# Optimization experiments

Measured on AMD Instinct MI355X. Metric: run time of the kernel, lower is better.

## Reference

```python
import jax, jax.numpy as jnp
import numpy as np

I, H, L, O = 128, 512, 2, 1  # input_size, hidden_size, num_layers, output_size
B, S = 64, 512


def setup_inputs() -> dict:
    key = jax.random.key(0)
    ks = jax.random.split(key, 12)
    inp = {
        "x": jax.random.normal(ks[0], (B, S, I), dtype=jnp.float32),
        "theta": jax.random.normal(ks[1], (I, H), dtype=jnp.float32) * 0.02,
        "phi": jax.random.normal(ks[2], (I, H), dtype=jnp.float32) * 0.02,
        "theta_noise": jax.random.normal(ks[3], (I, H), dtype=jnp.float32) * 0.01,
        "phi_noise": jax.random.normal(ks[4], (I, H), dtype=jnp.float32) * 0.01,
        # stacked per-layer LSTM weights (all layers take H-dim input)
        "W_ih": jax.random.normal(ks[5], (L, 4 * H, H), dtype=jnp.float32) * (1.0 / np.sqrt(H)),
        "W_hh": jax.random.normal(ks[6], (L, 4 * H, H), dtype=jnp.float32) * (1.0 / np.sqrt(H)),
        "b_ih": jax.random.normal(ks[7], (L, 4 * H), dtype=jnp.float32) * (1.0 / np.sqrt(H)),
        "b_hh": jax.random.normal(ks[8], (L, 4 * H), dtype=jnp.float32) * (1.0 / np.sqrt(H)),
        "fc1_w": jax.random.normal(ks[9], (H, H), dtype=jnp.float32) * (1.0 / np.sqrt(H)),
        "fc1_b": jnp.zeros((H,), dtype=jnp.float32),
        "fc2_w": jax.random.normal(ks[10], (O, H), dtype=jnp.float32) * (1.0 / np.sqrt(H)),
        "fc2_b": jnp.zeros((O,), dtype=jnp.float32),
    }
    return inp


def _lstm_layer(xs, Wih, Whh, bih, bhh):
    # xs: (S, B, H) -> hs: (S, B, H). PyTorch gate order: i, f, g, o.
    Bn = xs.shape[1]
    Hn = Whh.shape[1]
    # precompute input projections for all timesteps in one GEMM
    x_proj = jnp.einsum("sbh,gh->sbg", xs, Wih) + bih + bhh  # (S, B, 4H)

    def step(carry, xp):
        h, c = carry
        gates = xp + h @ Whh.T  # (B, 4H)
        i, f, g, o = jnp.split(gates, 4, axis=-1)
        i = jax.nn.sigmoid(i)
        f = jax.nn.sigmoid(f)
        g = jnp.tanh(g)
        o = jax.nn.sigmoid(o)
        c = f * c + i * g
        h = o * jnp.tanh(c)
        return (h, c), h

    h0 = jnp.zeros((Bn, Hn), dtype=xs.dtype)
    c0 = jnp.zeros((Bn, Hn), dtype=xs.dtype)
    _, hs = jax.lax.scan(step, (h0, c0), x_proj)
    return hs


def reference(x, theta, phi, theta_noise, phi_noise, W_ih, W_hh, b_ih, b_hh,
              fc1_w, fc1_b, fc2_w, fc2_b):
    # QuantumInspiredLayer: |x @ (cos(theta+n) + i*sin(phi+n))| done as two real GEMMs
    real = jnp.einsum("bsi,ih->bsh", x, jnp.cos(theta + theta_noise))
    imag = jnp.einsum("bsi,ih->bsh", x, jnp.sin(phi + phi_noise))
    q = jnp.sqrt(real * real + imag * imag)  # (B, S, H)

    hs = jnp.transpose(q, (1, 0, 2))  # (S, B, H)
    n_layers = W_ih.shape[0]
    for l in range(n_layers):
        hs = _lstm_layer(hs, W_ih[l], W_hh[l], b_ih[l], b_hh[l])
    last = hs[-1]  # (B, H) -- out[:, -1, :]

    h1 = jax.nn.relu(last @ fc1_w.T + fc1_b)
    # dropout is identity in eval mode
    return h1 @ fc2_w.T + fc2_b  # (B, O)
```

## Files before the change

kernel.cpp:

```cpp
#include <hip/hip_runtime.h>


typedef _Float16 f16;
typedef _Float16 f16x8 __attribute__((ext_vector_type(8)));
typedef float f32x4 __attribute__((ext_vector_type(4)));
typedef unsigned long long u64;

#define MFMA16(a, b, c) __builtin_amdgcn_mfma_f32_16x16x32_f16((a), (b), (c), 0, 0, 0)
#define LD_AG(p) __hip_atomic_load((p), __ATOMIC_RELAXED, __HIP_MEMORY_SCOPE_AGENT)
#define ST_AG(p, v) __hip_atomic_store((p), (v), __ATOMIC_RELAXED, __HIP_MEMORY_SCOPE_AGENT)

#define OFF_Q16 0UL
#define OFF_X16 33554432UL
#define OFF_W16 41943040UL
#define OFF_COS 50331648UL
#define OFF_SIN 50462720UL
#define OFF_BSUM 50593792UL
#define OFF_HBUF 50610176UL
#define OFF_HLAST 51003392UL
#define OFF_FC1WT 51134464UL
#define OFF_FLG 52183040UL
#define WS_NEEDED 52215808UL

__global__ __launch_bounds__(256) void k_prep(
    const float* __restrict__ x, const float* __restrict__ theta,
    const float* __restrict__ phi, const float* __restrict__ thn,
    const float* __restrict__ phn, const float* __restrict__ Wih,
    const float* __restrict__ Whh, const float* __restrict__ bih,
    const float* __restrict__ bhh, const float* __restrict__ fc1w,
    f16* __restrict__ x16, f16* __restrict__ w16, f16* __restrict__ cosT,
    f16* __restrict__ sinT, float* __restrict__ bsum, float* __restrict__ fc1wT,
    f16* __restrict__ hbuf, unsigned* __restrict__ flg) {
  const int T1 = 4194304;
  const int T2 = T1 + 4194304;
  const int T3 = T2 + 65536;
  const int T4 = T3 + 262144;
  const int T5 = T4 + 4096;
  const int T6 = T5 + 196608;
  const int T7 = T6 + 8192;
  for (int idx = blockIdx.x * 256 + threadIdx.x; idx < T7; idx += gridDim.x * 256) {
    if (idx < T1) {
      int s = idx >> 13, rem = idx & 8191, b = rem >> 7, i = rem & 127;
      x16[idx] = (f16)x[b * 65536 + s * 128 + i];
    } else if (idx < T2) {
      int j = idx - T1;
      int l = j >> 21, rem = j & 2097151, r = rem >> 10, k = rem & 1023;
      float v = (k < 512) ? Wih[((size_t)l * 2048 + r) * 512 + k]
                          : Whh[((size_t)l * 2048 + r) * 512 + (k - 512)];
      w16[(size_t)l * 2097152 + (size_t)r * 1024 + k] = (f16)v;
    } else if (idx < T3) {
      int e = idx - T2;
      int i = e >> 9, h = e & 511;
      cosT[h * 128 + i] = (f16)cosf(theta[e] + thn[e]);
      sinT[h * 128 + i] = (f16)sinf(phi[e] + phn[e]);
    } else if (idx < T4) {
      int e = idx - T3;
      int n = e >> 9, k = e & 511;
      fc1wT[k * 512 + n] = fc1w[e];
    } else if (idx < T5) {
      int e = idx - T4;
      bsum[e] = bih[e] + bhh[e];
    } else if (idx < T6) {
      hbuf[idx - T5] = (f16)0.f;
    } else {
      flg[idx - T6] = 0u;
    }
  }
}

__global__ __launch_bounds__(256) void k_quantum(
    const f16* __restrict__ x16, const f16* __restrict__ cosT,
    const f16* __restrict__ sinT, f16* __restrict__ q16) {
  __shared__ __align__(16) f16 a_lds[64 * 136];
  const int tid = threadIdx.x;
  const int r0 = blockIdx.x * 64, h0 = blockIdx.y * 128;
#pragma unroll
  for (int g = 0; g < 4; ++g) {
    int G = g * 256 + tid, row = G >> 4, col = G & 15;
    *(uint4*)((char*)a_lds + row * 272 + col * 16) =
        *(const uint4*)(x16 + (size_t)(r0 + row) * 128 + col * 8);
  }
  __syncthreads();
  const int wv = tid >> 6, lane = tid & 63, n15 = lane & 15, quad = lane >> 4;
  const int nb = h0 + wv * 32;
  f32x4 ac[4][2], as_[4][2];
#pragma unroll
  for (int mt = 0; mt < 4; ++mt)
#pragma unroll
    for (int nt = 0; nt < 2; ++nt) {
      ac[mt][nt] = (f32x4){0.f, 0.f, 0.f, 0.f};
      as_[mt][nt] = (f32x4){0.f, 0.f, 0.f, 0.f};
    }
#pragma unroll
  for (int it = 0; it < 4; ++it) {
    f16x8 a[4];
#pragma unroll
    for (int mt = 0; mt < 4; ++mt)
      a[mt] = *(const f16x8*)((const char*)a_lds + (mt * 16 + n15) * 272 + it * 64 + quad * 16);
#pragma unroll
    for (int nt = 0; nt < 2; ++nt) {
      const f16x8 bc = *(const f16x8*)(cosT + (size_t)(nb + nt * 16 + n15) * 128 + it * 32 + quad * 8);
      const f16x8 bs = *(const f16x8*)(sinT + (size_t)(nb + nt * 16 + n15) * 128 + it * 32 + quad * 8);
#pragma unroll
      for (int mt = 0; mt < 4; ++mt) {
        ac[mt][nt] = MFMA16(a[mt], bc, ac[mt][nt]);
        as_[mt][nt] = MFMA16(a[mt], bs, as_[mt][nt]);
      }
    }
  }
#pragma unroll
  for (int mt = 0; mt < 4; ++mt)
#pragma unroll
    for (int nt = 0; nt < 2; ++nt)
#pragma unroll
      for (int r = 0; r < 4; ++r) {
        int row = r0 + mt * 16 + quad * 4 + r;
        int col = nb + nt * 16 + n15;
        float re = ac[mt][nt][r], im = as_[mt][nt][r];
        q16[(size_t)row * 512 + col] = (f16)sqrtf(re * re + im * im);
      }
}

__device__ __forceinline__ f16x8 lds_a(const char* astage, int row, int it, int quad) {
  int pos = (it * 4 + quad) ^ (row & 7);
  return *(const f16x8*)(astage + row * 2048 + pos * 16);
}
__device__ __forceinline__ float sigf(float x) { return 1.f / (1.f + __expf(-x)); }
__device__ __forceinline__ float tanhf_fast(float x) { return 1.f - 2.f / (__expf(2.f * x) + 1.f); }

__global__ __launch_bounds__(512, 2) void k_rec(
    const f16* __restrict__ q16, const f16* __restrict__ w16,
    const float* __restrict__ bsum, f16* __restrict__ h0buf,
    f16* __restrict__ h1buf, float* __restrict__ hlast, unsigned* flg) {
  __shared__ __align__(16) char astage[32768];
  __shared__ float gbuf[16 * 132];

  const int tid = threadIdx.x, lane = tid & 63, wv = tid >> 6;
  const int n15 = lane & 15, quad = lane >> 4;
  const int qg = wv >> 1, ch = wv & 1;
  const int dom = blockIdx.x >> 5, role = blockIdx.x & 31;
  const int l = role >> 4, c0 = (role & 15) * 32;
  const int b0 = dom * 16;

  f16x8 wf[32];
  {
    const f16* wbase = w16 + ((size_t)l * 2048 + (size_t)(qg * 512 + c0 + ch * 16 + n15)) * 1024 + quad * 8;
#pragma unroll
    for (int it = 0; it < 32; ++it) wf[it] = *(const f16x8*)(wbase + it * 32);
  }
  float bb[4][2];
#pragma unroll
  for (int g = 0; g < 4; ++g)
#pragma unroll
    for (int j = 0; j < 2; ++j)
      bb[g][j] = bsum[l * 2048 + g * 512 + c0 + (tid & 15) * 2 + j];
  float cs0 = 0.f, cs1 = 0.f;

  unsigned* f0 = flg + (size_t)(dom * 2 + 0) * 1024;
  unsigned* f1 = flg + (size_t)(dom * 2 + 1) * 1024;
  unsigned* myflag = (l ? f1 : f0) + (size_t)(role & 15) * 64;
  const int pl = lane & 31;
  const unsigned* pollp = (pl < 16) ? (f0 + pl * 64) : (f1 + (pl - 16) * 64);

  const int srow = tid >> 5, scg = tid & 31;
  const int g0 = scg * 2;
  char* a_x0 = astage + srow * 2048 + ((g0 ^ (srow & 7)) * 16);
  char* a_x1 = astage + srow * 2048 + (((g0 + 1) ^ (srow & 7)) * 16);
  char* a_h0 = a_x0 + 1024;
  char* a_h1 = a_x1 + 1024;
  const size_t soff = (size_t)srow * 512 + scg * 16;
  const size_t h0base = (size_t)dom * 4 * 8192;
  const size_t h1base = (size_t)dom * 2 * 8192;

  for (int t = 0; t <= 511; ++t) {
    if (l == 0) {
      const f16* src = q16 + ((size_t)(t * 64 + b0 + srow)) * 512 + scg * 16;
      uint4 v0 = *(const uint4*)src;
      uint4 v1 = *(const uint4*)(src + 8);
      *(uint4*)a_x0 = v0;
      *(uint4*)a_x1 = v1;
    }
    if (t >= 1 || l == 1) {
      const int mytgt = (l == 0) ? ((pl < 16) ? t : (t - 2))
                                 : ((pl < 16) ? (t + 1) : t);
      while (true) {
        int f = (int)LD_AG(pollp);
        if (__all(f >= mytgt)) break;
        __builtin_amdgcn_s_sleep(1);
      }
    }
    if (l == 0) {
      const u64* hs0 = (const u64*)(h0buf + h0base + (size_t)((t - 1) & 3) * 8192 + soff);
      u64 x0 = LD_AG(hs0);
      u64 x1 = LD_AG(hs0 + 1);
      u64 x2 = LD_AG(hs0 + 2);
      u64 x3 = LD_AG(hs0 + 3);
      ((u64*)a_h0)[0] = x0; ((u64*)a_h0)[1] = x1;
      ((u64*)a_h1)[0] = x2; ((u64*)a_h1)[1] = x3;
    } else {
      const u64* hs0 = (const u64*)(h0buf + h0base + (size_t)(t & 3) * 8192 + soff);
      u64 x0 = LD_AG(hs0);
      u64 x1 = LD_AG(hs0 + 1);
      u64 x2 = LD_AG(hs0 + 2);
      u64 x3 = LD_AG(hs0 + 3);
      const u64* hs1 = (const u64*)(h1buf + h1base + (size_t)((t - 1) & 1) * 8192 + soff);
      u64 y0 = LD_AG(hs1);
      u64 y1 = LD_AG(hs1 + 1);
      u64 y2 = LD_AG(hs1 + 2);
      u64 y3 = LD_AG(hs1 + 3);
      ((u64*)a_x0)[0] = x0; ((u64*)a_x0)[1] = x1;
      ((u64*)a_x1)[0] = x2; ((u64*)a_x1)[1] = x3;
      ((u64*)a_h0)[0] = y0; ((u64*)a_h0)[1] = y1;
      ((u64*)a_h1)[0] = y2; ((u64*)a_h1)[1] = y3;
    }
    __syncthreads();

    f32x4 acc = (f32x4){0.f, 0.f, 0.f, 0.f};
#pragma unroll
    for (int it = 0; it < 32; ++it)
      acc = MFMA16(lds_a(astage, n15, it, quad), wf[it], acc);
#pragma unroll
    for (int r = 0; r < 4; ++r)
      gbuf[(quad * 4 + r) * 132 + qg * 33 + ch * 16 + n15] = acc[r];
    __syncthreads();

    if (tid < 256) {
      const int b = tid >> 4, jc = (tid & 15) * 2;
      float hv[2];
#pragma unroll
      for (int j = 0; j < 2; ++j) {
        const float* gb = gbuf + b * 132 + jc + j;
        float gi = gb[0] + bb[0][j];
        float gf = gb[33] + bb[1][j];
        float gg = gb[66] + bb[2][j];
        float go = gb[99] + bb[3][j];
        float cprev = j ? cs1 : cs0;
        float c = sigf(gf) * cprev + sigf(gi) * tanhf_fast(gg);
        if (j) cs1 = c; else cs0 = c;
        hv[j] = sigf(go) * tanhf_fast(c);
      }
      union { f16 h2[2]; unsigned u; } pk;
      pk.h2[0] = (f16)hv[0];
      pk.h2[1] = (f16)hv[1];
      f16* dst = (l == 0)
          ? h0buf + h0base + (size_t)(t & 3) * 8192 + (size_t)b * 512 + c0 + jc
          : h1buf + h1base + (size_t)(t & 1) * 8192 + (size_t)b * 512 + c0 + jc;
      ST_AG((unsigned*)dst, pk.u);
      if (l == 1 && t == 511) {
        hlast[(size_t)(b0 + b) * 512 + c0 + jc] = hv[0];
        hlast[(size_t)(b0 + b) * 512 + c0 + jc + 1] = hv[1];
      }
    }
    __syncthreads();
    if (tid == 0) ST_AG(myflag, (unsigned)(t + 1));
  }
}

__global__ __launch_bounds__(512) void k_fc(
    const float* __restrict__ hlast, const float* __restrict__ fc1wT,
    const float* __restrict__ fc1b, const float* __restrict__ fc2w,
    const float* __restrict__ fc2b, float* __restrict__ out) {
  __shared__ float hrow[512];
  __shared__ float red[8];
  const int b = blockIdx.x, tid = threadIdx.x;
  hrow[tid] = hlast[b * 512 + tid];
  __syncthreads();
  float acc = 0.f;
#pragma unroll 8
  for (int k = 0; k < 512; ++k) acc += hrow[k] * fc1wT[k * 512 + tid];
  float h1 = acc + fc1b[tid];
  h1 = h1 > 0.f ? h1 : 0.f;
  float v = h1 * fc2w[tid];
#pragma unroll
  for (int off = 32; off >= 1; off >>= 1) v += __shfl_down(v, off);
  if ((tid & 63) == 0) red[tid >> 6] = v;
  __syncthreads();
  if (tid == 0) {
    float s = 0.f;
#pragma unroll
    for (int w = 0; w < 8; ++w) s += red[w];
    out[b] = s + fc2b[0];
  }
}

extern "C" void kernel_launch(void* const* d_in, const int* in_sizes, int n_in,
                              void* d_out, int out_size, void* d_ws, size_t ws_size,
                              hipStream_t stream) {
  if (ws_size < WS_NEEDED) return;

  const float* x = (const float*)d_in[0];
  const float* theta = (const float*)d_in[1];
  const float* phi = (const float*)d_in[2];
  const float* thn = (const float*)d_in[3];
  const float* phn = (const float*)d_in[4];
  const float* Wih = (const float*)d_in[5];
  const float* Whh = (const float*)d_in[6];
  const float* bih = (const float*)d_in[7];
  const float* bhh = (const float*)d_in[8];
  const float* fc1w = (const float*)d_in[9];
  const float* fc1b = (const float*)d_in[10];
  const float* fc2w = (const float*)d_in[11];
  const float* fc2b = (const float*)d_in[12];

  char* ws = (char*)d_ws;
  f16* q16 = (f16*)(ws + OFF_Q16);
  f16* x16 = (f16*)(ws + OFF_X16);
  f16* w16 = (f16*)(ws + OFF_W16);
  f16* cosT = (f16*)(ws + OFF_COS);
  f16* sinT = (f16*)(ws + OFF_SIN);
  float* bsum = (float*)(ws + OFF_BSUM);
  f16* h0buf = (f16*)(ws + OFF_HBUF);
  f16* h1buf = h0buf + 131072;
  float* hlast = (float*)(ws + OFF_HLAST);
  float* fc1wT = (float*)(ws + OFF_FC1WT);
  unsigned* flg = (unsigned*)(ws + OFF_FLG);

  k_prep<<<2048, 256, 0, stream>>>(x, theta, phi, thn, phn, Wih, Whh, bih, bhh, fc1w,
                                   x16, w16, cosT, sinT, bsum, fc1wT, h0buf, flg);
  k_quantum<<<dim3(512, 4, 1), 256, 0, stream>>>(x16, cosT, sinT, q16);
  k_rec<<<128, 512, 0, stream>>>(q16, w16, bsum, h0buf, h1buf, hlast, flg);
  k_fc<<<64, 512, 0, stream>>>(hlast, fc1wT, fc1b, fc2w, fc2b, (float*)d_out);
}
```

Baseline: 1.860 ms.

## Replace flag-based sync with data-sentinel polling in persistent LSTM kernel

Per-block progress flags plus a trailing barrier are replaced by polling the hidden-state buffers themselves, with 0xFFFF sentinels marking slots not yet written. Ring buffers grow to 8 slots for layer 0 and 4 for layer 1, and writers invalidate a future slot after each step. A single flag from layer 1 throttles layer 0 so it cannot overrun the ring. Block-to-role mapping is changed so that each domain/layer pair shares an XCD, and the MFMA chain is split into two accumulators for more instruction-level parallelism. The aim is to cut the round-trip latency of flag writes and the extra barrier on each timestep. The risk is correctness if an fp16 value ever equals the sentinel pattern (NaN bits) or if memory ordering between value stores and sentinel resets breaks.

Result: slower. 2.151 ms (+15.7%).

```diff
diff --git a/kernel.cpp b/kernel.cpp
--- a/kernel.cpp
+++ b/kernel.cpp
@@ -17,10 +17,10 @@
 #define OFF_SIN 50462720UL
 #define OFF_BSUM 50593792UL
 #define OFF_HBUF 50610176UL
-#define OFF_HLAST 51003392UL
-#define OFF_FC1WT 51134464UL
-#define OFF_FLG 52183040UL
-#define WS_NEEDED 52215808UL
+#define OFF_HLAST 51396608UL
+#define OFF_FC1WT 51527680UL
+#define OFF_FLG 52576256UL
+#define WS_NEEDED 52609024UL
 
 __global__ __launch_bounds__(256) void k_prep(
     const float* __restrict__ x, const float* __restrict__ theta,
@@ -36,7 +36,7 @@
   const int T3 = T2 + 65536;
   const int T4 = T3 + 262144;
   const int T5 = T4 + 4096;
-  const int T6 = T5 + 196608;
+  const int T6 = T5 + 393216;
   const int T7 = T6 + 8192;
   for (int idx = blockIdx.x * 256 + threadIdx.x; idx < T7; idx += gridDim.x * 256) {
     if (idx < T1) {
@@ -61,7 +61,16 @@
       int e = idx - T4;
       bsum[e] = bih[e] + bhh[e];
     } else if (idx < T6) {
-      hbuf[idx - T5] = (f16)0.f;
+      int e = idx - T5;
+      unsigned short v;
+      if (e < 262144) {
+        int slot = (e >> 13) & 7;
+        v = (slot == 7) ? (unsigned short)0 : (unsigned short)0xFFFFu;
+      } else {
+        int slot = ((e - 262144) >> 13) & 3;
+        v = (slot == 3) ? (unsigned short)0 : (unsigned short)0xFFFFu;
+      }
+      ((unsigned short*)hbuf)[e] = v;
     } else {
       flg[idx - T6] = 0u;
     }
@@ -127,6 +136,12 @@
 }
 __device__ __forceinline__ float sigf(float x) { return 1.f / (1.f + __expf(-x)); }
 __device__ __forceinline__ float tanhf_fast(float x) { return 1.f - 2.f / (__expf(2.f * x) + 1.f); }
+__device__ __forceinline__ int v8ok(u64 a, u64 b, u64 c, u64 d) {
+  return ((unsigned)a != ~0u) & ((unsigned)(a >> 32) != ~0u) &
+         ((unsigned)b != ~0u) & ((unsigned)(b >> 32) != ~0u) &
+         ((unsigned)c != ~0u) & ((unsigned)(c >> 32) != ~0u) &
+         ((unsigned)d != ~0u) & ((unsigned)(d >> 32) != ~0u);
+}
 
 __global__ __launch_bounds__(512, 2) void k_rec(
     const f16* __restrict__ q16, const f16* __restrict__ w16,
@@ -138,8 +153,9 @@
   const int tid = threadIdx.x, lane = tid & 63, wv = tid >> 6;
   const int n15 = lane & 15, quad = lane >> 4;
   const int qg = wv >> 1, ch = wv & 1;
-  const int dom = blockIdx.x >> 5, role = blockIdx.x & 31;
-  const int l = role >> 4, c0 = (role & 15) * 32;
+  const int xcd = blockIdx.x & 7;
+  const int dom = xcd >> 1, l = xcd & 1, cg = blockIdx.x >> 3;
+  const int c0 = cg * 32;
   const int b0 = dom * 16;
 
   f16x8 wf[32];
@@ -156,11 +172,9 @@
       bb[g][j] = bsum[l * 2048 + g * 512 + c0 + (tid & 15) * 2 + j];
   float cs0 = 0.f, cs1 = 0.f;
 
-  unsigned* f0 = flg + (size_t)(dom * 2 + 0) * 1024;
-  unsigned* f1 = flg + (size_t)(dom * 2 + 1) * 1024;
-  unsigned* myflag = (l ? f1 : f0) + (size_t)(role & 15) * 64;
-  const int pl = lane & 31;
-  const unsigned* pollp = (pl < 16) ? (f0 + pl * 64) : (f1 + (pl - 16) * 64);
+  unsigned* f1dom = flg + (size_t)dom * 1024;
+  unsigned* myflag = f1dom + (size_t)cg * 64;
+  const unsigned* f1p = f1dom + (size_t)(lane & 15) * 64;
 
   const int srow = tid >> 5, scg = tid & 31;
   const int g0 = scg * 2;
@@ -169,8 +183,8 @@
   char* a_h0 = a_x0 + 1024;
   char* a_h1 = a_x1 + 1024;
   const size_t soff = (size_t)srow * 512 + scg * 16;
-  const size_t h0base = (size_t)dom * 4 * 8192;
-  const size_t h1base = (size_t)dom * 2 * 8192;
+  const size_t h0base = (size_t)dom * 8 * 8192;
+  const size_t h1base = (size_t)dom * 4 * 8192;
 
   for (int t = 0; t <= 511; ++t) {
     if (l == 0) {
@@ -179,46 +193,49 @@
       uint4 v1 = *(const uint4*)(src + 8);
       *(uint4*)a_x0 = v0;
       *(uint4*)a_x1 = v1;
-    }
-    if (t >= 1 || l == 1) {
-      const int mytgt = (l == 0) ? ((pl < 16) ? t : (t - 2))
-                                 : ((pl < 16) ? (t + 1) : t);
+      const u64* hs = (const u64*)(h0buf + h0base + (size_t)((t - 1) & 7) * 8192 + soff);
+      u64 x0, x1, x2, x3;
       while (true) {
-        int f = (int)LD_AG(pollp);
-        if (__all(f >= mytgt)) break;
+        x0 = LD_AG(hs); x1 = LD_AG(hs + 1); x2 = LD_AG(hs + 2); x3 = LD_AG(hs + 3);
+        unsigned fv = LD_AG(f1p);
+        int ok = v8ok(x0, x1, x2, x3) & ((int)fv >= t - 5);
+        if (__all(ok)) break;
         __builtin_amdgcn_s_sleep(1);
       }
-    }
-    if (l == 0) {
-      const u64* hs0 = (const u64*)(h0buf + h0base + (size_t)((t - 1) & 3) * 8192 + soff);
-      u64 x0 = LD_AG(hs0);
-      u64 x1 = LD_AG(hs0 + 1);
-      u64 x2 = LD_AG(hs0 + 2);
-      u64 x3 = LD_AG(hs0 + 3);
       ((u64*)a_h0)[0] = x0; ((u64*)a_h0)[1] = x1;
       ((u64*)a_h1)[0] = x2; ((u64*)a_h1)[1] = x3;
     } else {
-      const u64* hs0 = (const u64*)(h0buf + h0base + (size_t)(t & 3) * 8192 + soff);
-      u64 x0 = LD_AG(hs0);
-      u64 x1 = LD_AG(hs0 + 1);
-      u64 x2 = LD_AG(hs0 + 2);
-      u64 x3 = LD_AG(hs0 + 3);
-      const u64* hs1 = (const u64*)(h1buf + h1base + (size_t)((t - 1) & 1) * 8192 + soff);
-      u64 y0 = LD_AG(hs1);
-      u64 y1 = LD_AG(hs1 + 1);
-      u64 y2 = LD_AG(hs1 + 2);
-      u64 y3 = LD_AG(hs1 + 3);
+      const u64* hs1 = (const u64*)(h1buf + h1base + (size_t)((t - 1) & 3) * 8192 + soff);
+      u64 y0, y1, y2, y3;
+      while (true) {
+        y0 = LD_AG(hs1); y1 = LD_AG(hs1 + 1); y2 = LD_AG(hs1 + 2); y3 = LD_AG(hs1 + 3);
+        if (__all(v8ok(y0, y1, y2, y3))) break;
+        __builtin_amdgcn_s_sleep(1);
+      }
+      ((u64*)a_h0)[0] = y0; ((u64*)a_h0)[1] = y1;
+      ((u64*)a_h1)[0] = y2; ((u64*)a_h1)[1] = y3;
+      const u64* hs0 = (const u64*)(h0buf + h0base + (size_t)(t & 7) * 8192 + soff);
+      u64 x0, x1, x2, x3;
+      while (true) {
+        x0 = LD_AG(hs0); x1 = LD_AG(hs0 + 1); x2 = LD_AG(hs0 + 2); x3 = LD_AG(hs0 + 3);
+        if (__all(v8ok(x0, x1, x2, x3))) break;
+        __builtin_amdgcn_s_sleep(1);
+      }
       ((u64*)a_x0)[0] = x0; ((u64*)a_x0)[1] = x1;
       ((u64*)a_x1)[0] = x2; ((u64*)a_x1)[1] = x3;
-      ((u64*)a_h0)[0] = y0; ((u64*)a_h0)[1] = y1;
-      ((u64*)a_h1)[0] = y2; ((u64*)a_h1)[1] = y3;
     }
     __syncthreads();
 
-    f32x4 acc = (f32x4){0.f, 0.f, 0.f, 0.f};
-#pragma unroll
-    for (int it = 0; it < 32; ++it)
-      acc = MFMA16(lds_a(astage, n15, it, quad), wf[it], acc);
+    if (l == 1 && tid == 0) ST_AG(myflag, (unsigned)(t + 1));
+
+    f32x4 acc0 = (f32x4){0.f, 0.f, 0.f, 0.f};
+    f32x4 acc1 = (f32x4){0.f, 0.f, 0.f, 0.f};
+#pragma unroll
+    for (int it = 0; it < 32; it += 2) {
+      acc0 = MFMA16(lds_a(astage, n15, it, quad), wf[it], acc0);
+      acc1 = MFMA16(lds_a(astage, n15, it + 1, quad), wf[it + 1], acc1);
+    }
+    f32x4 acc = acc0 + acc1;
 #pragma unroll
     for (int r = 0; r < 4; ++r)
       gbuf[(quad * 4 + r) * 132 + qg * 33 + ch * 16 + n15] = acc[r];
@@ -242,17 +259,24 @@
       union { f16 h2[2]; unsigned u; } pk;
       pk.h2[0] = (f16)hv[0];
       pk.h2[1] = (f16)hv[1];
-      f16* dst = (l == 0)
-          ? h0buf + h0base + (size_t)(t & 3) * 8192 + (size_t)b * 512 + c0 + jc
-          : h1buf + h1base + (size_t)(t & 1) * 8192 + (size_t)b * 512 + c0 + jc;
-      ST_AG((unsigned*)dst, pk.u);
-      if (l == 1 && t == 511) {
-        hlast[(size_t)(b0 + b) * 512 + c0 + jc] = hv[0];
-        hlast[(size_t)(b0 + b) * 512 + c0 + jc + 1] = hv[1];
-      }
-    }
-    __syncthreads();
-    if (tid == 0) ST_AG(myflag, (unsigned)(t + 1));
+      if (l == 0) {
+        f16* dst = h0buf + h0base + (size_t)(t & 7) * 8192 + (size_t)b * 512 + c0 + jc;
+        ST_AG((unsigned*)dst, pk.u);
+        unsigned* fl = (unsigned*)(h0buf + h0base + (size_t)((t + 2) & 7) * 8192 +
+                                   (size_t)b * 512 + c0 + jc);
+        ST_AG(fl, ~0u);
+      } else {
+        f16* dst = h1buf + h1base + (size_t)(t & 3) * 8192 + (size_t)b * 512 + c0 + jc;
+        ST_AG((unsigned*)dst, pk.u);
+        unsigned* fl = (unsigned*)(h1buf + h1base + (size_t)((t + 2) & 3) * 8192 +
+                                   (size_t)b * 512 + c0 + jc);
+        ST_AG(fl, ~0u);
+        if (t == 511) {
+          hlast[(size_t)(b0 + b) * 512 + c0 + jc] = hv[0];
+          hlast[(size_t)(b0 + b) * 512 + c0 + jc + 1] = hv[1];
+        }
+      }
+    }
   }
 }
 
@@ -310,7 +334,7 @@
   f16* sinT = (f16*)(ws + OFF_SIN);
   float* bsum = (float*)(ws + OFF_BSUM);
   f16* h0buf = (f16*)(ws + OFF_HBUF);
-  f16* h1buf = h0buf + 131072;
+  f16* h1buf = h0buf + 262144;
   float* hlast = (float*)(ws + OFF_HLAST);
   float* fc1wT = (float*)(ws + OFF_FC1WT);
   unsigned* flg = (unsigned*)(ws + OFF_FLG);
```

## Overlap half-step MFMA with flag polling in LSTM recurrence and interleave block mapping

Applied to the files above, without the earlier changes.

Splits each timestep's gate GEMM into two K-halves so the half whose operand is already available (the x projection for layer 0, the own-layer h for layer 1) runs before waiting on the cross-block flag for the other half. This hides some of the spin-wait latency behind MFMA work. It also uses two accumulators to break the MFMA dependency chain, and remaps blockIdx so the batch-domain index is the low bits. A poll iteration cap is added as a deadlock guard, and it adds extra __syncthreads per step.

Measured after the change: 1.908 ms. 1.03x slower.

```diff
diff --git a/kernel.cpp b/kernel.cpp
--- a/kernel.cpp
+++ b/kernel.cpp
@@ -9,6 +9,7 @@
 #define MFMA16(a, b, c) __builtin_amdgcn_mfma_f32_16x16x32_f16((a), (b), (c), 0, 0, 0)
 #define LD_AG(p) __hip_atomic_load((p), __ATOMIC_RELAXED, __HIP_MEMORY_SCOPE_AGENT)
 #define ST_AG(p, v) __hip_atomic_store((p), (v), __ATOMIC_RELAXED, __HIP_MEMORY_SCOPE_AGENT)
+#define POLL_CAP (1 << 20)
 
 #define OFF_Q16 0UL
 #define OFF_X16 33554432UL
@@ -138,7 +139,7 @@
   const int tid = threadIdx.x, lane = tid & 63, wv = tid >> 6;
   const int n15 = lane & 15, quad = lane >> 4;
   const int qg = wv >> 1, ch = wv & 1;
-  const int dom = blockIdx.x >> 5, role = blockIdx.x & 31;
+  const int dom = blockIdx.x & 3, role = blockIdx.x >> 2;
   const int l = role >> 4, c0 = (role & 15) * 32;
   const int b0 = dom * 16;
 
@@ -161,6 +162,8 @@
   unsigned* myflag = (l ? f1 : f0) + (size_t)(role & 15) * 64;
   const int pl = lane & 31;
   const unsigned* pollp = (pl < 16) ? (f0 + pl * 64) : (f1 + (pl - 16) * 64);
+  const unsigned* pollf0 = f0 + (size_t)(lane & 15) * 64;
+  const unsigned* pollf1 = f1 + (size_t)(lane & 15) * 64;
 
   const int srow = tid >> 5, scg = tid & 31;
   const int g0 = scg * 2;
@@ -172,24 +175,33 @@
   const size_t h0base = (size_t)dom * 4 * 8192;
   const size_t h1base = (size_t)dom * 2 * 8192;
 
+  int alive = 1;
+
   for (int t = 0; t <= 511; ++t) {
+    f32x4 acc0 = (f32x4){0.f, 0.f, 0.f, 0.f};
+    f32x4 acc1 = (f32x4){0.f, 0.f, 0.f, 0.f};
     if (l == 0) {
       const f16* src = q16 + ((size_t)(t * 64 + b0 + srow)) * 512 + scg * 16;
       uint4 v0 = *(const uint4*)src;
       uint4 v1 = *(const uint4*)(src + 8);
       *(uint4*)a_x0 = v0;
       *(uint4*)a_x1 = v1;
-    }
-    if (t >= 1 || l == 1) {
-      const int mytgt = (l == 0) ? ((pl < 16) ? t : (t - 2))
-                                 : ((pl < 16) ? (t + 1) : t);
-      while (true) {
-        int f = (int)LD_AG(pollp);
-        if (__all(f >= mytgt)) break;
-        __builtin_amdgcn_s_sleep(1);
-      }
-    }
-    if (l == 0) {
+      __syncthreads();
+#pragma unroll
+      for (int it = 0; it < 16; it += 2) {
+        acc0 = MFMA16(lds_a(astage, n15, it, quad), wf[it], acc0);
+        acc1 = MFMA16(lds_a(astage, n15, it + 1, quad), wf[it + 1], acc1);
+      }
+      if (t >= 1 && alive) {
+        const int mytgt = (pl < 16) ? t : (t - 2);
+        int iters = 0;
+        while (true) {
+          int f = (int)LD_AG(pollp);
+          if (__all(f >= mytgt)) break;
+          if (++iters > POLL_CAP) { alive = 0; break; }
+          __builtin_amdgcn_s_sleep(1);
+        }
+      }
       const u64* hs0 = (const u64*)(h0buf + h0base + (size_t)((t - 1) & 3) * 8192 + soff);
       u64 x0 = LD_AG(hs0);
       u64 x1 = LD_AG(hs0 + 1);
@@ -197,28 +209,59 @@
       u64 x3 = LD_AG(hs0 + 3);
       ((u64*)a_h0)[0] = x0; ((u64*)a_h0)[1] = x1;
       ((u64*)a_h1)[0] = x2; ((u64*)a_h1)[1] = x3;
+      __syncthreads();
+#pragma unroll
+      for (int it = 16; it < 32; it += 2) {
+        acc0 = MFMA16(lds_a(astage, n15, it, quad), wf[it], acc0);
+        acc1 = MFMA16(lds_a(astage, n15, it + 1, quad), wf[it + 1], acc1);
+      }
     } else {
+      if (alive) {
+        int iters = 0;
+        while (true) {
+          int f = (int)LD_AG(pollf1);
+          if (__all(f >= t)) break;
+          if (++iters > POLL_CAP) { alive = 0; break; }
+          __builtin_amdgcn_s_sleep(1);
+        }
+      }
+      const u64* hs1 = (const u64*)(h1buf + h1base + (size_t)((t - 1) & 1) * 8192 + soff);
+      u64 y0 = LD_AG(hs1);
+      u64 y1 = LD_AG(hs1 + 1);
+      u64 y2 = LD_AG(hs1 + 2);
+      u64 y3 = LD_AG(hs1 + 3);
+      ((u64*)a_h0)[0] = y0; ((u64*)a_h0)[1] = y1;
+      ((u64*)a_h1)[0] = y2; ((u64*)a_h1)[1] = y3;
+      __syncthreads();
+#pragma unroll
+      for (int it = 16; it < 32; it += 2) {
+        acc0 = MFMA16(lds_a(astage, n15, it, quad), wf[it], acc0);
+        acc1 = MFMA16(lds_a(astage, n15, it + 1, quad), wf[it + 1], acc1);
+      }
+      if (alive) {
+        int iters = 0;
+        while (true) {
+          int f = (int)LD_AG(pollf0);
+          if (__all(f >= t + 1)) break;
+          if (++iters > POLL_CAP) { alive = 0; break; }
+          __builtin_amdgcn_s_sleep(1);
+        }
+      }
       const u64* hs0 = (const u64*)(h0buf + h0base + (size_t)(t & 3) * 8192 + soff);
       u64 x0 = LD_AG(hs0);
       u64 x1 = LD_AG(hs0 + 1);
       u64 x2 = LD_AG(hs0 + 2);
       u64 x3 = LD_AG(hs0 + 3);
-      const u64* hs1 = (const u64*)(h1buf + h1base + (size_t)((t - 1) & 1) * 8192 + soff);
-      u64 y0 = LD_AG(hs1);
-      u64 y1 = LD_AG(hs1 + 1);
-      u64 y2 = LD_AG(hs1 + 2);
-      u64 y3 = LD_AG(hs1 + 3);
       ((u64*)a_x0)[0] = x0; ((u64*)a_x0)[1] = x1;
       ((u64*)a_x1)[0] = x2; ((u64*)a_x1)[1] = x3;
-      ((u64*)a_h0)[0] = y0; ((u64*)a_h0)[1] = y1;
-      ((u64*)a_h1)[0] = y2; ((u64*)a_h1)[1] = y3;
-    }
-    __syncthreads();
-
-    f32x4 acc = (f32x4){0.f, 0.f, 0.f, 0.f};
-#pragma unroll
-    for (int it = 0; it < 32; ++it)
-      acc = MFMA16(lds_a(astage, n15, it, quad), wf[it], acc);
+      __syncthreads();
+#pragma unroll
+      for (int it = 0; it < 16; it += 2) {
+        acc0 = MFMA16(lds_a(astage, n15, it, quad), wf[it], acc0);
+        acc1 = MFMA16(lds_a(astage, n15, it + 1, quad), wf[it + 1], acc1);
+      }
+    }
+    f32x4 acc = acc0 + acc1;
 #pragma unroll
     for (int r = 0; r < 4; ++r)
       gbuf[(quad * 4 + r) * 132 + qg * 33 + ch * 16 + n15] = acc[r];
```

## Fuse LSTM gate math in-register via shuffles, deepen h0 ring, remap blocks

Applied to the files above, without the earlier changes.

The recurrent kernel now permutes weight rows so that each wave's MFMA output holds all four gates for its columns. Gate values are exchanged with lane shuffles instead of an LDS gbuf round-trip and a second __syncthreads, and the cell math is spread over all waves. The layer-0 hidden ring grows from 4 to 8 slots, letting layer 0 run up to 6 steps ahead of layer 1, and block-to-domain mapping is interleaved. Two accumulators split the MFMA dependency chain, and a poll cap prevents infinite spinning at the cost of possibly silent wrong results if it triggers.

Result: slower. 2.197 ms (+18.1%).

```diff
diff --git a/kernel.cpp b/kernel.cpp
--- a/kernel.cpp
+++ b/kernel.cpp
@@ -9,6 +9,7 @@
 #define MFMA16(a, b, c) __builtin_amdgcn_mfma_f32_16x16x32_f16((a), (b), (c), 0, 0, 0)
 #define LD_AG(p) __hip_atomic_load((p), __ATOMIC_RELAXED, __HIP_MEMORY_SCOPE_AGENT)
 #define ST_AG(p, v) __hip_atomic_store((p), (v), __ATOMIC_RELAXED, __HIP_MEMORY_SCOPE_AGENT)
+#define POLL_CAP (1 << 20)
 
 #define OFF_Q16 0UL
 #define OFF_X16 33554432UL
@@ -17,10 +18,10 @@
 #define OFF_SIN 50462720UL
 #define OFF_BSUM 50593792UL
 #define OFF_HBUF 50610176UL
-#define OFF_HLAST 51003392UL
-#define OFF_FC1WT 51134464UL
-#define OFF_FLG 52183040UL
-#define WS_NEEDED 52215808UL
+#define OFF_HLAST 51265536UL
+#define OFF_FC1WT 51396608UL
+#define OFF_FLG 52445184UL
+#define WS_NEEDED 52477952UL
 
 __global__ __launch_bounds__(256) void k_prep(
     const float* __restrict__ x, const float* __restrict__ theta,
@@ -36,7 +37,7 @@
   const int T3 = T2 + 65536;
   const int T4 = T3 + 262144;
   const int T5 = T4 + 4096;
-  const int T6 = T5 + 196608;
+  const int T6 = T5 + 327680;
   const int T7 = T6 + 8192;
   for (int idx = blockIdx.x * 256 + threadIdx.x; idx < T7; idx += gridDim.x * 256) {
     if (idx < T1) {
@@ -133,32 +134,29 @@
     const float* __restrict__ bsum, f16* __restrict__ h0buf,
     f16* __restrict__ h1buf, float* __restrict__ hlast, unsigned* flg) {
   __shared__ __align__(16) char astage[32768];
-  __shared__ float gbuf[16 * 132];
 
   const int tid = threadIdx.x, lane = tid & 63, wv = tid >> 6;
   const int n15 = lane & 15, quad = lane >> 4;
-  const int qg = wv >> 1, ch = wv & 1;
-  const int dom = blockIdx.x >> 5, role = blockIdx.x & 31;
-  const int l = role >> 4, c0 = (role & 15) * 32;
+  const int dom = blockIdx.x & 3, role = blockIdx.x >> 2;
+  const int l = role >> 4, cg = role & 15, c0 = cg * 32;
   const int b0 = dom * 16;
 
   f16x8 wf[32];
   {
-    const f16* wbase = w16 + ((size_t)l * 2048 + (size_t)(qg * 512 + c0 + ch * 16 + n15)) * 1024 + quad * 8;
+    const int brow = (n15 >> 2) * 512 + c0 + wv * 4 + (n15 & 3);
+    const f16* wbase = w16 + ((size_t)l * 2048 + (size_t)brow) * 1024 + quad * 8;
 #pragma unroll
     for (int it = 0; it < 32; ++it) wf[it] = *(const f16x8*)(wbase + it * 32);
   }
-  float bb[4][2];
-#pragma unroll
-  for (int g = 0; g < 4; ++g)
-#pragma unroll
-    for (int j = 0; j < 2; ++j)
-      bb[g][j] = bsum[l * 2048 + g * 512 + c0 + (tid & 15) * 2 + j];
-  float cs0 = 0.f, cs1 = 0.f;
+  const int mycol = c0 + wv * 4 + (n15 & 3);
+  float bbv[4];
+#pragma unroll
+  for (int g = 0; g < 4; ++g) bbv[g] = bsum[l * 2048 + g * 512 + mycol];
+  float cstate[4] = {0.f, 0.f, 0.f, 0.f};
 
   unsigned* f0 = flg + (size_t)(dom * 2 + 0) * 1024;
   unsigned* f1 = flg + (size_t)(dom * 2 + 1) * 1024;
-  unsigned* myflag = (l ? f1 : f0) + (size_t)(role & 15) * 64;
+  unsigned* myflag = (l ? f1 : f0) + (size_t)cg * 64;
   const int pl = lane & 31;
   const unsigned* pollp = (pl < 16) ? (f0 + pl * 64) : (f1 + (pl - 16) * 64);
 
@@ -169,8 +167,10 @@
   char* a_h0 = a_x0 + 1024;
   char* a_h1 = a_x1 + 1024;
   const size_t soff = (size_t)srow * 512 + scg * 16;
-  const size_t h0base = (size_t)dom * 4 * 8192;
+  const size_t h0base = (size_t)dom * 8 * 8192;
   const size_t h1base = (size_t)dom * 2 * 8192;
+
+  int alive = 1;
 
   for (int t = 0; t <= 511; ++t) {
     if (l == 0) {
@@ -180,17 +180,19 @@
       *(uint4*)a_x0 = v0;
       *(uint4*)a_x1 = v1;
     }
-    if (t >= 1 || l == 1) {
-      const int mytgt = (l == 0) ? ((pl < 16) ? t : (t - 2))
+    if ((t >= 1 || l == 1) && alive) {
+      const int mytgt = (l == 0) ? ((pl < 16) ? t : (t - 6))
                                  : ((pl < 16) ? (t + 1) : t);
+      int iters = 0;
       while (true) {
         int f = (int)LD_AG(pollp);
         if (__all(f >= mytgt)) break;
+        if (++iters > POLL_CAP) { alive = 0; break; }
         __builtin_amdgcn_s_sleep(1);
       }
     }
     if (l == 0) {
-      const u64* hs0 = (const u64*)(h0buf + h0base + (size_t)((t - 1) & 3) * 8192 + soff);
+      const u64* hs0 = (const u64*)(h0buf + h0base + (size_t)((t - 1) & 7) * 8192 + soff);
       u64 x0 = LD_AG(hs0);
       u64 x1 = LD_AG(hs0 + 1);
       u64 x2 = LD_AG(hs0 + 2);
@@ -198,7 +200,7 @@
       ((u64*)a_h0)[0] = x0; ((u64*)a_h0)[1] = x1;
       ((u64*)a_h1)[0] = x2; ((u64*)a_h1)[1] = x3;
     } else {
-      const u64* hs0 = (const u64*)(h0buf + h0base + (size_t)(t & 3) * 8192 + soff);
+      const u64* hs0 = (const u64*)(h0buf + h0base + (size_t)(t & 7) * 8192 + soff);
       u64 x0 = LD_AG(hs0);
       u64 x1 = LD_AG(hs0 + 1);
       u64 x2 = LD_AG(hs0 + 2);
@@ -215,40 +217,42 @@
     }
     __syncthreads();
 
-    f32x4 acc = (f32x4){0.f, 0.f, 0.f, 0.f};
-#pragma unroll
-    for (int it = 0; it < 32; ++it)
-      acc = MFMA16(lds_a(astage, n15, it, quad), wf[it], acc);
-#pragma unroll
-    for (int r = 0; r < 4; ++r)
-      gbuf[(quad * 4 + r) * 132 + qg * 33 + ch * 16 + n15] = acc[r];
-    __syncthreads();
-
-    if (tid < 256) {
-      const int b = tid >> 4, jc = (tid & 15) * 2;
-      float hv[2];
-#pragma unroll
-      for (int j = 0; j < 2; ++j) {
-        const float* gb = gbuf + b * 132 + jc + j;
-        float gi = gb[0] + bb[0][j];
-        float gf = gb[33] + bb[1][j];
-        float gg = gb[66] + bb[2][j];
-        float go = gb[99] + bb[3][j];
-        float cprev = j ? cs1 : cs0;
-        float c = sigf(gf) * cprev + sigf(gi) * tanhf_fast(gg);
-        if (j) cs1 = c; else cs0 = c;
-        hv[j] = sigf(go) * tanhf_fast(c);
-      }
-      union { f16 h2[2]; unsigned u; } pk;
-      pk.h2[0] = (f16)hv[0];
-      pk.h2[1] = (f16)hv[1];
-      f16* dst = (l == 0)
-          ? h0buf + h0base + (size_t)(t & 3) * 8192 + (size_t)b * 512 + c0 + jc
-          : h1buf + h1base + (size_t)(t & 1) * 8192 + (size_t)b * 512 + c0 + jc;
-      ST_AG((unsigned*)dst, pk.u);
-      if (l == 1 && t == 511) {
-        hlast[(size_t)(b0 + b) * 512 + c0 + jc] = hv[0];
-        hlast[(size_t)(b0 + b) * 512 + c0 + jc + 1] = hv[1];
+    f32x4 acc0 = (f32x4){0.f, 0.f, 0.f, 0.f};
+    f32x4 acc1 = (f32x4){0.f, 0.f, 0.f, 0.f};
+#pragma unroll
+    for (int it = 0; it < 32; it += 2) {
+      acc0 = MFMA16(lds_a(astage, n15, it, quad), wf[it], acc0);
+      acc1 = MFMA16(lds_a(astage, n15, it + 1, quad), wf[it + 1], acc1);
+    }
+    f32x4 acc = acc0 + acc1;
+
+    float gfv[4], ggv[4], gov[4];
+#pragma unroll
+    for (int r = 0; r < 4; ++r) {
+      gfv[r] = __shfl(acc[r], lane + 4);
+      ggv[r] = __shfl(acc[r], lane + 8);
+      gov[r] = __shfl(acc[r], lane + 12);
+    }
+    if (n15 < 4) {
+#pragma unroll
+      for (int r = 0; r < 4; ++r) {
+        float gi_ = acc[r] + bbv[0];
+        float gf_ = gfv[r] + bbv[1];
+        float gg_ = ggv[r] + bbv[2];
+        float go_ = gov[r] + bbv[3];
+        float c = sigf(gf_) * cstate[r] + sigf(gi_) * tanhf_fast(gg_);
+        cstate[r] = c;
+        float hv = sigf(go_) * tanhf_fast(c);
+        union { f16 h; unsigned short u; } pk;
+        pk.h = (f16)hv;
+        const int row = quad * 4 + r;
+        unsigned short* dst = (l == 0)
+            ? (unsigned short*)(h0buf + h0base + (size_t)(t & 7) * 8192 + (size_t)row * 512 + mycol)
+            : (unsigned short*)(h1buf + h1base + (size_t)(t & 1) * 8192 + (size_t)row * 512 + mycol);
+        ST_AG(dst, pk.u);
+        if (l == 1 && t == 511) {
+          hlast[(size_t)(b0 + row) * 512 + mycol] = hv;
+        }
       }
     }
     __syncthreads();
@@ -310,7 +314,7 @@
   f16* sinT = (f16*)(ws + OFF_SIN);
   float* bsum = (float*)(ws + OFF_BSUM);
   f16* h0buf = (f16*)(ws + OFF_HBUF);
-  f16* h1buf = h0buf + 131072;
+  f16* h1buf = h0buf + 262144;
   float* hlast = (float*)(ws + OFF_HLAST);
   float* fc1wT = (float*)(ws + OFF_FC1WT);
   unsigned* flg = (unsigned*)(ws + OFF_FLG);
```
